# Kernel tuning notes

Hardware: AMD Instinct MI355X
Metric: run time of the kernel (lower is better)

Reference implementation:

```python
import jax, jax.numpy as jnp
import numpy as np

B, N, H, V, STEP = 16, 50, 128, 40000, 2

def setup_inputs() -> dict:
    key = jax.random.key(0)
    ks = jax.random.split(key, 24)
    def nrm(i, shape, s=0.08):
        return jax.random.normal(ks[i], shape, jnp.float32) * s
    items = jax.random.randint(ks[0], (B, N), 0, V)
    A = jax.random.uniform(ks[1], (B, N, 2 * N), jnp.float32)
    lengths = jax.random.randint(ks[2], (B,), 1, N + 1)
    mask = (jnp.arange(N)[None, :] < lengths[:, None]).astype(jnp.int32)
    emb = nrm(3, (V, H), 0.1).at[0].set(0.0)  # padding_idx=0 row zeroed
    return dict(
        items=items, A=A, mask=mask, emb=emb,
        w_ih=nrm(4, (3 * H, 2 * H)), w_hh=nrm(5, (3 * H, H)),
        b_ih=nrm(6, (3 * H,)), b_hh=nrm(7, (3 * H,)),
        b_iah=nrm(8, (H,)), b_oah=nrm(9, (H,)),
        W_ein=nrm(10, (H, H)), b_ein=nrm(11, (H,)),
        W_eout=nrm(12, (H, H)), b_eout=nrm(13, (H,)),
        W_one=nrm(14, (H, H)), b_one=nrm(15, (H,)),
        W_two=nrm(16, (H, H)), b_two=nrm(17, (H,)),
        w_three=nrm(18, (H,)),
        W_tr=nrm(19, (H, 2 * H)), b_tr=nrm(20, (H,)),
        W_t=nrm(21, (H, H)),
    )

def gnn_cell(A, hidden, w_ih, w_hh, b_ih, b_hh, b_iah, b_oah, W_ein, b_ein, W_eout, b_eout):
    # A: [B,N,2N], hidden: [B,N,H]
    ein = hidden @ W_ein.T + b_ein
    eout = hidden @ W_eout.T + b_eout
    input_in = jnp.einsum('bnm,bmh->bnh', A[:, :, :N], ein) + b_iah
    input_out = jnp.einsum('bnm,bmh->bnh', A[:, :, N:], eout) + b_oah
    inputs = jnp.concatenate([input_in, input_out], axis=-1)  # [B,N,2H]
    gi = inputs @ w_ih.T + b_ih
    gh = hidden @ w_hh.T + b_hh
    i_r, i_i, i_n = jnp.split(gi, 3, axis=-1)
    h_r, h_i, h_n = jnp.split(gh, 3, axis=-1)
    resetgate = jax.nn.sigmoid(i_r + h_r)
    inputgate = jax.nn.sigmoid(i_i + h_i)
    newgate = jnp.tanh(i_n + resetgate * h_n)
    return newgate + inputgate * (hidden - newgate)

def reference(items, A, mask, emb, w_ih, w_hh, b_ih, b_hh, b_iah, b_oah,
              W_ein, b_ein, W_eout, b_eout, W_one, b_one, W_two, b_two,
              w_three, W_tr, b_tr, W_t):
    hidden = emb[items]  # [B,N,H]
    for _ in range(STEP):
        hidden = gnn_cell(A, hidden, w_ih, w_hh, b_ih, b_hh, b_iah, b_oah,
                          W_ein, b_ein, W_eout, b_eout)
    # compute_scores
    lengths = jnp.sum(mask, axis=1)  # all >= 1 by construction
    ht = hidden[jnp.arange(B), lengths - 1]  # [B,H] last valid item
    q1 = (ht @ W_one.T + b_one)[:, None, :]
    q2 = hidden @ W_two.T + b_two
    mexp = mask[..., None].astype(jnp.float32)  # [B,N,1]
    alpha_logits = jax.nn.sigmoid(q1 + q2) @ w_three[:, None]  # [B,N,1]
    alpha = jax.nn.softmax(jnp.where(mexp == 0, -jnp.inf, alpha_logits), axis=1)
    a = jnp.sum(alpha * hidden * mexp, axis=1)  # [B,H]
    a = jnp.concatenate([a, ht], axis=1) @ W_tr.T + b_tr  # hybrid (nonhybrid=False)
    b_emb = emb[1:]  # [V-1,H]
    qt = (hidden * mexp) @ W_t.T  # [B,N,H]
    beta_logits = jnp.einsum('vh,bnh->bvn', b_emb, qt)
    beta_logits = jnp.where(mask[:, None, :] == 0, -jnp.inf, beta_logits)
    beta = jax.nn.softmax(beta_logits, axis=-1)  # [B,V-1,N]
    target = jnp.einsum('bvn,bnh->bvh', beta, qt * mexp)  # [B,V-1,H]
    # scores = sum((a[:,None,:] + target) * b_emb, -1), split to avoid extra buffer
    scores = jnp.einsum('bvh,vh->bv', target, b_emb) + a @ b_emb.T
    return scores  # [B, V-1]
```

## Files before the change

### kernel.cpp

```cpp
#include <hip/hip_runtime.h>

#define BB 16
#define NN 50
#define HH 128
#define VV 40000
#define VO 39999

typedef unsigned short u16;
typedef unsigned int u32;
typedef __attribute__((ext_vector_type(8))) short short8;
typedef __attribute__((ext_vector_type(4))) float f32x4;

#define OFF_HID    0
#define OFF_EIN    102400
#define OFF_Q2     102400
#define OFF_EOUT   204800
#define OFF_Q1     204800
#define OFF_HT     206848
#define OFF_QTBF   307200
#define OFF_LEN    411648
#define OFF_WIHT   411664
#define OFF_WHHT   509968
#define OFF_WEINT  559120
#define OFF_WEOUTT 575504
#define OFF_WTWOT  591888
#define OFF_WTT    608272
#define OFF_WONET  624656
#define OFF_WTRT   641040

__device__ __forceinline__ float sigm(float x){ return 1.0f/(1.0f+__expf(-x)); }
__device__ __forceinline__ float b2f(u16 u){
  union { u32 i; float f; } c; c.i = ((u32)u) << 16; return c.f;
}
__device__ __forceinline__ u16 f2b(float f){
  union { float f; u32 i; } c; c.f = f;
  u32 u = c.i;
  return (u16)((u + 0x7fffu + ((u >> 16) & 1u)) >> 16);
}
__device__ __forceinline__ int frag_idx(int b, int n, int k){
  int tile = n>>4, vlo = n&15, kc = k>>5, quad = (k>>3)&3, j = k&7;
  return (((b*4+tile)*4+kc)<<9) + ((quad<<4)+vlo)*8 + j;
}

__global__ void k_pre(const int* __restrict__ items, const float* __restrict__ emb,
                      const float* __restrict__ w_ih, const float* __restrict__ w_hh,
                      const float* __restrict__ W_ein, const float* __restrict__ W_eout,
                      const float* __restrict__ W_two, const float* __restrict__ W_t,
                      const float* __restrict__ W_one, const float* __restrict__ W_tr,
                      float* __restrict__ ws){
  int idx = blockIdx.x*256 + threadIdx.x;
  if (idx < 102400){
    int r = idx >> 7, h = idx & 127;
    ws[OFF_HID + idx] = emb[items[r]*128 + h];
  } else if (idx < 200704){
    int i = idx-102400; int k=i/384, j=i-k*384;
    ws[OFF_WIHT + i] = w_ih[j*256 + k];
  } else if (idx < 249856){
    int i = idx-200704; int k=i/384, j=i-k*384;
    ws[OFF_WHHT + i] = w_hh[j*128 + k];
  } else if (idx < 266240){
    int i = idx-249856; int k=i>>7, h=i&127;
    ws[OFF_WEINT + i] = W_ein[h*128 + k];
  } else if (idx < 282624){
    int i = idx-266240; int k=i>>7, h=i&127;
    ws[OFF_WEOUTT + i] = W_eout[h*128 + k];
  } else if (idx < 299008){
    int i = idx-282624; int k=i>>7, h=i&127;
    ws[OFF_WTWOT + i] = W_two[h*128 + k];
  } else if (idx < 315392){
    int i = idx-299008; int k=i>>7, h=i&127;
    ws[OFF_WTT + i] = W_t[h*128 + k];
  } else if (idx < 331776){
    int i = idx-315392; int k=i>>7, h=i&127;
    ws[OFF_WONET + i] = W_one[h*128 + k];
  } else if (idx < 364544){
    int i = idx-331776; int k=i>>7, h=i&127;
    ws[OFF_WTRT + i] = W_tr[h*256 + k];
  }
}

__global__ void __launch_bounds__(256) k_einout(const float* __restrict__ b_ein,
                         const float* __restrict__ b_eout, float* __restrict__ ws){
  __shared__ float hl[256];
  int t = threadIdx.x;
  int r0 = blockIdx.x * 2;
  hl[t] = ws[OFF_HID + r0*128 + t];
  __syncthreads();
  int h = t & 127;
  const float* wT = ws + ((t<128) ? OFF_WEINT : OFF_WEOUTT);
  float bias = ((t<128)? b_ein : b_eout)[h];
  float a0 = bias, a1 = bias;
  for (int k=0;k<128;k+=4){
    float w0 = wT[(k+0)*128+h], w1 = wT[(k+1)*128+h];
    float w2 = wT[(k+2)*128+h], w3 = wT[(k+3)*128+h];
    float4 h0 = *(const float4*)(hl + k);
    float4 h1 = *(const float4*)(hl + 128 + k);
    a0 += h0.x*w0 + h0.y*w1 + h0.z*w2 + h0.w*w3;
    a1 += h1.x*w0 + h1.y*w1 + h1.z*w2 + h1.w*w3;
  }
  float* dst = ws + ((t<128) ? OFF_EIN : OFF_EOUT);
  dst[(r0+0)*128 + h] = a0;
  dst[(r0+1)*128 + h] = a1;
}

__global__ void __launch_bounds__(384) k_cell(const float* __restrict__ A,
                       const float* __restrict__ b_iah, const float* __restrict__ b_oah,
                       const float* __restrict__ b_ih, const float* __restrict__ b_hh,
                       float* __restrict__ ws){
  __shared__ float hidr[4][128];
  __shared__ float arow[4][104];
  __shared__ float inp[4][256];
  __shared__ float gil[4][384];
  __shared__ float ghl[4][384];
  int t = threadIdx.x;
  int tile = blockIdx.x, b = blockIdx.y;
  int n0 = tile*4;
  for (int o=t; o<512; o+=384){
    int r=o>>7, h=o&127, row=n0+r;
    hidr[r][h] = (row<NN) ? ws[OFF_HID + (b*NN+row)*128 + h] : 0.0f;
  }
  for (int o=t; o<416; o+=384){
    int r=o/104, c=o-r*104;
    arow[r][c] = (c<100 && n0+r<NN) ? A[(size_t)(b*NN+n0+r)*100 + c] : 0.0f;
  }
  __syncthreads();
  for (int o=t; o<1024; o+=384){
    int r = o>>8, c8 = o&255;
    int half = (c8 < 128) ? 1 : 0;
    int c = c8 & 127;
    int row = n0 + r;
    float acc = 0.0f;
    if (row < NN){
      acc = half ? b_iah[c] : b_oah[c];
      const float* src = ws + (half?OFF_EIN:OFF_EOUT) + b*6400 + c;
      const float* ar = &arow[r][half?0:50];
      #pragma unroll 5
      for (int m=0;m<50;m++) acc += ar[m] * src[m*128];
    }
    inp[r][c8] = acc;
  }
  __syncthreads();
  {
    int j = t;
    float gi[4], gh[4];
    float bi = b_ih[j], bh = b_hh[j];
    #pragma unroll
    for (int r=0;r<4;r++){ gi[r]=bi; gh[r]=bh; }
    const float* wti = ws + OFF_WIHT;
    const float* wth = ws + OFF_WHHT;
    for (int k=0;k<256;k+=4){
      float w0 = wti[(k+0)*384+j], w1 = wti[(k+1)*384+j];
      float w2 = wti[(k+2)*384+j], w3_ = wti[(k+3)*384+j];
      #pragma unroll
      for (int r=0;r<4;r++){
        float4 iv = *(const float4*)(&inp[r][k]);
        gi[r] += iv.x*w0 + iv.y*w1 + iv.z*w2 + iv.w*w3_;
      }
    }
    for (int k=0;k<128;k+=4){
      float w0 = wth[(k+0)*384+j], w1 = wth[(k+1)*384+j];
      float w2 = wth[(k+2)*384+j], w3_ = wth[(k+3)*384+j];
      #pragma unroll
      for (int r=0;r<4;r++){
        float4 hv = *(const float4*)(&hidr[r][k]);
        gh[r] += hv.x*w0 + hv.y*w1 + hv.z*w2 + hv.w*w3_;
      }
    }
    #pragma unroll
    for (int r=0;r<4;r++){ gil[r][j]=gi[r]; ghl[r][j]=gh[r]; }
  }
  __syncthreads();
  for (int o=t; o<512; o+=384){
    int r=o>>7, h=o&127, row=n0+r;
    if (row<NN){
      float ir_=gil[r][h], ii=gil[r][128+h], inw=gil[r][256+h];
      float hr_=ghl[r][h], hi=ghl[r][128+h], hn=ghl[r][256+h];
      float rg=sigm(ir_+hr_), ig=sigm(ii+hi), ng=tanhf(inw+rg*hn);
      float hv=hidr[r][h];
      ws[OFF_HID + (b*NN+row)*128 + h] = ng + ig*(hv-ng);
    }
  }
}

__global__ void __launch_bounds__(256) k_post(const int* __restrict__ mask,
                      const float* __restrict__ b_two, const float* __restrict__ b_one,
                      float* __restrict__ ws){
  int bx = blockIdx.x, t = threadIdx.x;
  u16* qtbf = (u16*)(ws + OFF_QTBF);
  if (bx < 200){
    bool isq2 = bx < 100;
    int r0 = (isq2 ? bx : bx-100) * 8;
    __shared__ float hl[1024];
    for (int i=0;i<4;i++) hl[t+i*256] = ws[OFF_HID + r0*128 + t + i*256];
    __syncthreads();
    int h = t & 127, g = t >> 7;
    const float* wT = ws + (isq2 ? OFF_WTWOT : OFF_WTT);
    float binit = isq2 ? b_two[h] : 0.0f;
    float acc[4];
    #pragma unroll
    for (int r=0;r<4;r++) acc[r] = binit;
    for (int k4=0;k4<32;k4++){
      int k = k4*4;
      float w0 = wT[(k+0)*128+h], w1 = wT[(k+1)*128+h];
      float w2 = wT[(k+2)*128+h], w3 = wT[(k+3)*128+h];
      #pragma unroll
      for (int r=0;r<4;r++){
        float4 hv = *(const float4*)(hl + (g*4+r)*128 + k);
        acc[r] += hv.x*w0 + hv.y*w1 + hv.z*w2 + hv.w*w3;
      }
    }
    #pragma unroll
    for (int r=0;r<4;r++){
      int row = r0 + g*4 + r;
      if (isq2) ws[OFF_Q2 + row*128 + h] = acc[r];
      else {
        float val = mask[row] ? acc[r] : 0.0f;
        int b = row/NN, n = row - b*NN;
        qtbf[frag_idx(b, n, h)] = f2b(val);
      }
    }
  } else if (bx < 248){
    int i = (bx-200)*256 + t;
    #pragma unroll
    for (int kk=0;kk<2;kk++){
      int e = i*2 + kk;
      int b = e/1536, rem = e - b*1536;
      int kc = rem/384, rem2 = rem - kc*384;
      int quad = rem2/96, vv = rem2 - quad*96;
      int vlo = 4 + vv/8, j = vv & 7;
      qtbf[(((b*4+3)*4+kc)<<9) + ((quad<<4)+vlo)*8 + j] = 0;
    }
  } else {
    __shared__ float htl[128];
    int b = bx - 248;
    if (t < 128){
      int len = 0;
      for (int n=0;n<NN;n++) len += mask[b*NN+n];
      if (len<1) len=1; if (len>NN) len=NN;
      float ht = ws[OFF_HID + (b*NN + len-1)*128 + t];
      ws[OFF_HT + b*128 + t] = ht;
      htl[t] = ht;
      if (t==0) ((int*)(ws+OFF_LEN))[b] = len;
    }
    __syncthreads();
    if (t < 128){
      const float* w1T = ws + OFF_WONET;
      float q1 = b_one[t];
      for (int k=0;k<128;k++) q1 += htl[k] * w1T[k*128 + t];
      ws[OFF_Q1 + b*128 + t] = q1;
    }
  }
}

__global__ void k_attn2(const float* __restrict__ w_three, const float* __restrict__ b_tr,
                        float* __restrict__ ws){
  __shared__ float q2l[NN*129];
  __shared__ float q1l[128], w3l[128], htl[128], al[128], alg[64];
  int t = threadIdx.x;
  int b = blockIdx.x;
  for (int o=t;o<NN*128;o+=128){ int n=o>>7, h=o&127; q2l[n*129+h] = ws[OFF_Q2 + b*NN*128 + o]; }
  q1l[t] = ws[OFF_Q1 + b*128 + t];
  w3l[t] = w_three[t];
  htl[t] = ws[OFF_HT + b*128 + t];
  int len = ((const int*)(ws+OFF_LEN))[b];
  __syncthreads();
  if (t < len){
    float s = 0.0f;
    const float* qr = q2l + t*129;
    for (int h=0;h<128;h++) s += w3l[h]*sigm(q1l[h]+qr[h]);
    alg[t] = s;
  }
  __syncthreads();
  if (t == 0){
    float mx = -1e30f;
    for (int n=0;n<len;n++) mx = fmaxf(mx, alg[n]);
    float ssum = 0.0f;
    for (int n=0;n<len;n++){ float e=__expf(alg[n]-mx); alg[n]=e; ssum+=e; }
    float inv = (ssum>0.0f)?1.0f/ssum:0.0f;
    for (int n=0;n<len;n++) alg[n]*=inv;
  }
  __syncthreads();
  const float* hid = ws + OFF_HID + b*NN*128;
  float a = 0.0f;
  for (int n=0;n<len;n++) a += alg[n]*hid[n*128+t];
  al[t] = a;
  __syncthreads();
  const float* wtr = ws + OFF_WTRT;
  float af = b_tr[t];
  for (int k=0;k<128;k++) af += al[k]  * wtr[k*128 + t];
  for (int k=0;k<128;k++) af += htl[k] * wtr[(128+k)*128 + t];
  u16 hi = f2b(af);
  u16 lo = f2b(af - b2f(hi));
  u16* qtbf = (u16*)(ws + OFF_QTBF);
  qtbf[frag_idx(b, 50, t)] = hi;
  qtbf[frag_idx(b, 51, t)] = lo;
}

__global__ void __launch_bounds__(256) k_scores(const float* __restrict__ emb,
                                                const float* __restrict__ ws,
                                                float* __restrict__ out){
  __shared__ u16 qlds[8192];
  int tid = threadIdx.x;
  int lane = tid & 63, wave = tid >> 6;
  int quad = lane >> 4, vlo = lane & 15;
  int v = blockIdx.x*64 + wave*16 + vlo;
  int vc = (v < VO) ? v : (VO-1);
  const float* erow = emb + (size_t)(vc+1)*128;
  short8 bfr[4];
  #pragma unroll
  for (int kc=0;kc<4;kc++){
    const float4* p = (const float4*)(erow + kc*32 + quad*8);
    float4 x = p[0], y = p[1];
    union { short8 s; u32 w[4]; } u;
    u.w[0] = (u32)f2b(x.x) | ((u32)f2b(x.y)<<16);
    u.w[1] = (u32)f2b(x.z) | ((u32)f2b(x.w)<<16);
    u.w[2] = (u32)f2b(y.x) | ((u32)f2b(y.y)<<16);
    u.w[3] = (u32)f2b(y.z) | ((u32)f2b(y.w)<<16);
    bfr[kc] = u.s;
  }
  const u16* qtf = (const u16*)(ws + OFF_QTBF);
  const int* slen = (const int*)(ws + OFF_LEN);
  int b0 = blockIdx.y*4;
  for (int bi=0;bi<4;bi++){
    int b = b0 + bi;
    __syncthreads();
    {
      const uint4* src = (const uint4*)qtf + (size_t)b*1024;
      uint4* dst = (uint4*)qlds;
      #pragma unroll
      for (int r=0;r<4;r++) dst[tid + r*256] = src[tid + r*256];
    }
    __syncthreads();
    int len = slen[b];
    f32x4 acc0={0.f,0.f,0.f,0.f}, acc1=acc0, acc2=acc0, acc3=acc0;
    #pragma unroll
    for (int kc=0;kc<4;kc++){
      const u16* base = qlds + kc*512 + lane*8;
      short8 a0 = *(const short8*)(base + 0*2048);
      short8 a1 = *(const short8*)(base + 1*2048);
      short8 a2 = *(const short8*)(base + 2*2048);
      short8 a3 = *(const short8*)(base + 3*2048);
      acc0 = __builtin_amdgcn_mfma_f32_16x16x32_bf16(a0, bfr[kc], acc0, 0,0,0);
      acc1 = __builtin_amdgcn_mfma_f32_16x16x32_bf16(a1, bfr[kc], acc1, 0,0,0);
      acc2 = __builtin_amdgcn_mfma_f32_16x16x32_bf16(a2, bfr[kc], acc2, 0,0,0);
      acc3 = __builtin_amdgcn_mfma_f32_16x16x32_bf16(a3, bfr[kc], acc3, 0,0,0);
    }
    int nb = quad*4;
    float ss=0.f, nm=0.f;
    #pragma unroll
    for (int r=0;r<4;r++){
      { int n=nb+r;    if(n<len){ float e=__expf(acc0[r]); ss+=e; nm+=e*acc0[r]; } }
      { int n=nb+r+16; if(n<len){ float e=__expf(acc1[r]); ss+=e; nm+=e*acc1[r]; } }
      { int n=nb+r+32; if(n<len){ float e=__expf(acc2[r]); ss+=e; nm+=e*acc2[r]; } }
      { int n=nb+r+48; if(n<len){ float e=__expf(acc3[r]); ss+=e; nm+=e*acc3[r]; } }
    }
    ss += __shfl_xor(ss,16); ss += __shfl_xor(ss,32);
    nm += __shfl_xor(nm,16); nm += __shfl_xor(nm,32);
    if (quad==0 && v < VO){
      float pa = acc3[2] + acc3[3];
      out[(size_t)b*VO + v] = nm/ss + pa;
    }
  }
}

extern "C" void kernel_launch(void* const* d_in, const int* in_sizes, int n_in,
                              void* d_out, int out_size, void* d_ws, size_t ws_size,
                              hipStream_t stream){
  const int*   items  = (const int*)d_in[0];
  const float* A      = (const float*)d_in[1];
  const int*   mask   = (const int*)d_in[2];
  const float* emb    = (const float*)d_in[3];
  const float* w_ih   = (const float*)d_in[4];
  const float* w_hh   = (const float*)d_in[5];
  const float* b_ih   = (const float*)d_in[6];
  const float* b_hh   = (const float*)d_in[7];
  const float* b_iah  = (const float*)d_in[8];
  const float* b_oah  = (const float*)d_in[9];
  const float* W_ein  = (const float*)d_in[10];
  const float* b_ein  = (const float*)d_in[11];
  const float* W_eout = (const float*)d_in[12];
  const float* b_eout = (const float*)d_in[13];
  const float* W_one  = (const float*)d_in[14];
  const float* b_one  = (const float*)d_in[15];
  const float* W_two  = (const float*)d_in[16];
  const float* b_two  = (const float*)d_in[17];
  const float* w_three= (const float*)d_in[18];
  const float* W_tr   = (const float*)d_in[19];
  const float* b_tr   = (const float*)d_in[20];
  const float* W_t    = (const float*)d_in[21];
  float* ws  = (float*)d_ws;
  float* out = (float*)d_out;

  k_pre<<<1424,256,0,stream>>>(items,emb,w_ih,w_hh,W_ein,W_eout,W_two,W_t,W_one,W_tr,ws);
  for (int s=0;s<2;s++){
    k_einout<<<400,256,0,stream>>>(b_ein,b_eout,ws);
    k_cell  <<<dim3(13,16),384,0,stream>>>(A,b_iah,b_oah,b_ih,b_hh,ws);
  }
  k_post <<<264,256,0,stream>>>(mask,b_two,b_one,ws);
  k_attn2<<<16,128,0,stream>>>(w_three,b_tr,ws);
  k_scores<<<dim3(625,4),256,0,stream>>>(emb,ws,out);
}
```

Measured before the change: 219.1 us.

## Fuse post-projection and attention kernels into one tail kernel, swap score grid axes

```diff
diff --git a/kernel.cpp b/kernel.cpp
--- a/kernel.cpp
+++ b/kernel.cpp
@@ -13,10 +13,7 @@
 
 #define OFF_HID    0
 #define OFF_EIN    102400
-#define OFF_Q2     102400
 #define OFF_EOUT   204800
-#define OFF_Q1     204800
-#define OFF_HT     206848
 #define OFF_QTBF   307200
 #define OFF_LEN    411648
 #define OFF_WIHT   411664
@@ -182,23 +179,26 @@
   }
 }
 
-__global__ void __launch_bounds__(256) k_post(const int* __restrict__ mask,
+__global__ void __launch_bounds__(256) k_tail(const int* __restrict__ mask,
                       const float* __restrict__ b_two, const float* __restrict__ b_one,
+                      const float* __restrict__ w_three, const float* __restrict__ b_tr,
                       float* __restrict__ ws){
+  __shared__ float hl[1024];
+  __shared__ float hidL[6400];
+  __shared__ float q2l[NN*129];
+  __shared__ float q1l[128], w3l[128], htl[128], al[128], alg[64], parts[256];
+  __shared__ int slen_s;
   int bx = blockIdx.x, t = threadIdx.x;
   u16* qtbf = (u16*)(ws + OFF_QTBF);
-  if (bx < 200){
-    bool isq2 = bx < 100;
-    int r0 = (isq2 ? bx : bx-100) * 8;
-    __shared__ float hl[1024];
+  if (bx < 100){
+    int r0 = bx * 8;
     for (int i=0;i<4;i++) hl[t+i*256] = ws[OFF_HID + r0*128 + t + i*256];
     __syncthreads();
     int h = t & 127, g = t >> 7;
-    const float* wT = ws + (isq2 ? OFF_WTWOT : OFF_WTT);
-    float binit = isq2 ? b_two[h] : 0.0f;
+    const float* wT = ws + OFF_WTT;
     float acc[4];
     #pragma unroll
-    for (int r=0;r<4;r++) acc[r] = binit;
+    for (int r=0;r<4;r++) acc[r] = 0.0f;
     for (int k4=0;k4<32;k4++){
       int k = k4*4;
       float w0 = wT[(k+0)*128+h], w1 = wT[(k+1)*128+h];
@@ -212,15 +212,12 @@
     #pragma unroll
     for (int r=0;r<4;r++){
       int row = r0 + g*4 + r;
-      if (isq2) ws[OFF_Q2 + row*128 + h] = acc[r];
-      else {
-        float val = mask[row] ? acc[r] : 0.0f;
-        int b = row/NN, n = row - b*NN;
-        qtbf[frag_idx(b, n, h)] = f2b(val);
-      }
-    }
-  } else if (bx < 248){
-    int i = (bx-200)*256 + t;
+      float val = mask[row] ? acc[r] : 0.0f;
+      int b = row/NN, n = row - b*NN;
+      qtbf[frag_idx(b, n, h)] = f2b(val);
+    }
+  } else if (bx < 148){
+    int i = (bx-100)*256 + t;
     #pragma unroll
     for (int kk=0;kk<2;kk++){
       int e = i*2 + kk;
@@ -231,69 +228,80 @@
       qtbf[(((b*4+3)*4+kc)<<9) + ((quad<<4)+vlo)*8 + j] = 0;
     }
   } else {
-    __shared__ float htl[128];
-    int b = bx - 248;
-    if (t < 128){
+    int b = bx - 148;
+    for (int o=t; o<6400; o+=256) hidL[o] = ws[OFF_HID + b*6400 + o];
+    if (t == 0){
       int len = 0;
       for (int n=0;n<NN;n++) len += mask[b*NN+n];
       if (len<1) len=1; if (len>NN) len=NN;
-      float ht = ws[OFF_HID + (b*NN + len-1)*128 + t];
-      ws[OFF_HT + b*128 + t] = ht;
-      htl[t] = ht;
-      if (t==0) ((int*)(ws+OFF_LEN))[b] = len;
+      slen_s = len;
+      ((int*)(ws+OFF_LEN))[b] = len;
+    }
+    __syncthreads();
+    int len = slen_s;
+    if (t < 128){
+      htl[t] = hidL[(len-1)*128 + t];
+      w3l[t] = w_three[t];
     }
     __syncthreads();
     if (t < 128){
       const float* w1T = ws + OFF_WONET;
       float q1 = b_one[t];
       for (int k=0;k<128;k++) q1 += htl[k] * w1T[k*128 + t];
-      ws[OFF_Q1 + b*128 + t] = q1;
-    }
-  }
-}
-
-__global__ void k_attn2(const float* __restrict__ w_three, const float* __restrict__ b_tr,
-                        float* __restrict__ ws){
-  __shared__ float q2l[NN*129];
-  __shared__ float q1l[128], w3l[128], htl[128], al[128], alg[64];
-  int t = threadIdx.x;
-  int b = blockIdx.x;
-  for (int o=t;o<NN*128;o+=128){ int n=o>>7, h=o&127; q2l[n*129+h] = ws[OFF_Q2 + b*NN*128 + o]; }
-  q1l[t] = ws[OFF_Q1 + b*128 + t];
-  w3l[t] = w_three[t];
-  htl[t] = ws[OFF_HT + b*128 + t];
-  int len = ((const int*)(ws+OFF_LEN))[b];
-  __syncthreads();
-  if (t < len){
-    float s = 0.0f;
-    const float* qr = q2l + t*129;
-    for (int h=0;h<128;h++) s += w3l[h]*sigm(q1l[h]+qr[h]);
-    alg[t] = s;
-  }
-  __syncthreads();
-  if (t == 0){
-    float mx = -1e30f;
-    for (int n=0;n<len;n++) mx = fmaxf(mx, alg[n]);
-    float ssum = 0.0f;
-    for (int n=0;n<len;n++){ float e=__expf(alg[n]-mx); alg[n]=e; ssum+=e; }
-    float inv = (ssum>0.0f)?1.0f/ssum:0.0f;
-    for (int n=0;n<len;n++) alg[n]*=inv;
-  }
-  __syncthreads();
-  const float* hid = ws + OFF_HID + b*NN*128;
-  float a = 0.0f;
-  for (int n=0;n<len;n++) a += alg[n]*hid[n*128+t];
-  al[t] = a;
-  __syncthreads();
-  const float* wtr = ws + OFF_WTRT;
-  float af = b_tr[t];
-  for (int k=0;k<128;k++) af += al[k]  * wtr[k*128 + t];
-  for (int k=0;k<128;k++) af += htl[k] * wtr[(128+k)*128 + t];
-  u16 hi = f2b(af);
-  u16 lo = f2b(af - b2f(hi));
-  u16* qtbf = (u16*)(ws + OFF_QTBF);
-  qtbf[frag_idx(b, 50, t)] = hi;
-  qtbf[frag_idx(b, 51, t)] = lo;
+      q1l[t] = q1;
+    }
+    {
+      int c = t & 127, g = t >> 7;
+      const float* w2T = ws + OFF_WTWOT;
+      float bt2 = b_two[c];
+      for (int m=g; m<NN; m+=2){
+        float acc = bt2;
+        const float* hr = hidL + m*128;
+        for (int k=0;k<128;k+=4){
+          float4 hv = *(const float4*)(hr + k);
+          acc += hv.x*w2T[(k+0)*128+c] + hv.y*w2T[(k+1)*128+c]
+               + hv.z*w2T[(k+2)*128+c] + hv.w*w2T[(k+3)*128+c];
+        }
+        q2l[m*129 + c] = acc;
+      }
+    }
+    __syncthreads();
+    if (t < 200){
+      int r = t>>2, p = t&3;
+      float s = 0.0f;
+      const float* qr = q2l + r*129;
+      for (int h=p*32; h<p*32+32; h++) s += w3l[h]*sigm(q1l[h]+qr[h]);
+      parts[t] = s;
+    }
+    __syncthreads();
+    if (t < NN) alg[t] = parts[t*4]+parts[t*4+1]+parts[t*4+2]+parts[t*4+3];
+    __syncthreads();
+    if (t == 0){
+      float mx = -1e30f;
+      for (int n=0;n<len;n++) mx = fmaxf(mx, alg[n]);
+      float ssum = 0.0f;
+      for (int n=0;n<len;n++){ float e=__expf(alg[n]-mx); alg[n]=e; ssum+=e; }
+      float inv = (ssum>0.0f)?1.0f/ssum:0.0f;
+      for (int n=0;n<len;n++) alg[n]*=inv;
+    }
+    __syncthreads();
+    if (t < 128){
+      float a = 0.0f;
+      for (int n=0;n<len;n++) a += alg[n]*hidL[n*128+t];
+      al[t] = a;
+    }
+    __syncthreads();
+    if (t < 128){
+      const float* wtr = ws + OFF_WTRT;
+      float af = b_tr[t];
+      for (int k=0;k<128;k++) af += al[k]  * wtr[k*128 + t];
+      for (int k=0;k<128;k++) af += htl[k] * wtr[(128+k)*128 + t];
+      u16 hi = f2b(af);
+      u16 lo = f2b(af - b2f(hi));
+      qtbf[frag_idx(b, 50, t)] = hi;
+      qtbf[frag_idx(b, 51, t)] = lo;
+    }
+  }
 }
 
 __global__ void __launch_bounds__(256) k_scores(const float* __restrict__ emb,
@@ -303,7 +311,7 @@
   int tid = threadIdx.x;
   int lane = tid & 63, wave = tid >> 6;
   int quad = lane >> 4, vlo = lane & 15;
-  int v = blockIdx.x*64 + wave*16 + vlo;
+  int v = blockIdx.y*64 + wave*16 + vlo;
   int vc = (v < VO) ? v : (VO-1);
   const float* erow = emb + (size_t)(vc+1)*128;
   short8 bfr[4];
@@ -320,7 +328,7 @@
   }
   const u16* qtf = (const u16*)(ws + OFF_QTBF);
   const int* slen = (const int*)(ws + OFF_LEN);
-  int b0 = blockIdx.y*4;
+  int b0 = blockIdx.x*4;
   for (int bi=0;bi<4;bi++){
     int b = b0 + bi;
     __syncthreads();
@@ -396,7 +404,6 @@
     k_einout<<<400,256,0,stream>>>(b_ein,b_eout,ws);
     k_cell  <<<dim3(13,16),384,0,stream>>>(A,b_iah,b_oah,b_ih,b_hh,ws);
   }
-  k_post <<<264,256,0,stream>>>(mask,b_two,b_one,ws);
-  k_attn2<<<16,128,0,stream>>>(w_three,b_tr,ws);
-  k_scores<<<dim3(625,4),256,0,stream>>>(emb,ws,out);
-}
+  k_tail<<<164,256,0,stream>>>(mask,b_two,b_one,w_three,b_tr,ws);
+  k_scores<<<dim3(4,625),256,0,stream>>>(emb,ws,out);
+}
```

After: 228.5 us. 1.04x slower.
